# Kernel optimization log

Measured on AMD Instinct MI355X. Metric: run time of the kernel, lower is better.

## Reference

```python
import jax, jax.numpy as jnp
import numpy as np

# pywt db2 decomposition filters
DEC_LO = np.array([-0.12940952255092145, 0.22414386804185735,
                   0.8365163037378079, 0.4829629131445341], dtype=np.float32)
DEC_HI = np.array([-0.4829629131445341, 0.8365163037378079,
                   -0.22414386804185735, -0.12940952255092145], dtype=np.float32)
LEVEL = 3
REC_WEIGHT = 1.0
FILT_LEN = 4
PAD = (2 * FILT_LEN - 3) // 2  # = 2, ptwt reflect padding per side


def _filters(dtype):
    # ptwt uses cross-correlation with flipped pywt filters (== true convolution)
    lo = jnp.asarray(DEC_LO[::-1].copy(), dtype=dtype)
    hi = jnp.asarray(DEC_HI[::-1].copy(), dtype=dtype)
    ll = jnp.outer(lo, lo)  # 'a'
    lh = jnp.outer(hi, lo)  # 'h'
    hl = jnp.outer(lo, hi)  # 'v'
    hh = jnp.outer(hi, hi)  # 'd'
    return jnp.stack([ll, lh, hl, hh])[:, None]  # [4,1,4,4]


def _dwt_step(x, filt):
    # x: [N, nb, H, W] -> [N, 4*nb, H', W'] (each band split into a,h,v,d; grouped)
    n, nb, h, w = x.shape
    padb = PAD + (h % 2)
    padr = PAD + (w % 2)
    xp = jnp.pad(x, ((0, 0), (0, 0), (PAD, padb), (PAD, padr)), mode='reflect')
    k = jnp.tile(filt, (nb, 1, 1, 1))  # [4*nb, 1, 4, 4]
    return jax.lax.conv_general_dilated(
        xp, k, window_strides=(2, 2), padding='VALID',
        feature_group_count=nb,
        dimension_numbers=('NCHW', 'OIHW', 'NCHW'))


def setup_inputs() -> dict:
    key = jax.random.key(0)
    k1, k2 = jax.random.split(key)
    preds = jax.random.normal(k1, (64, 3, 512, 512), dtype=jnp.float32)
    targets = jax.random.normal(k2, (64, 3, 512, 512), dtype=jnp.float32)
    return {"preds": preds, "targets": targets}


def reference(preds, targets):
    n, c, h, w = preds.shape
    p = preds.reshape(n * c, 1, h, w)
    t = targets.reshape(n * c, 1, h, w)
    filt = _filters(preds.dtype)
    for _ in range(LEVEL):
        p = _dwt_step(p, filt)
        t = _dwt_step(t, filt)
    # p, t: [N*C, 4**LEVEL, h', w']; leaf 0 is the all-'a' (pure approx) packet
    per_leaf_mse = jnp.mean((p - t) ** 2, axis=(0, 2, 3))  # [4**LEVEL]
    wvec = jnp.ones(per_leaf_mse.shape[0], dtype=preds.dtype).at[0].set(0.5)
    return REC_WEIGHT * jnp.dot(wvec, per_leaf_mse)
```

## Files before the change

### kernel.cpp

```cpp
#include <hip/hip_runtime.h>

#define F_LO0 0.4829629131445341f
#define F_LO1 0.8365163037378079f
#define F_LO2 0.22414386804185735f
#define F_LO3 (-0.12940952255092145f)
#define F_HI0 (-0.12940952255092145f)
#define F_HI1 (-0.22414386804185735f)
#define F_HI2 0.8365163037378079f
#define F_HI3 (-0.4829629131445341f)

__device__ __forceinline__ int reflect_idx(int r, int n) {
    r = (r < 0) ? -r : r;
    r = (r >= n) ? 2 * n - 2 - r : r;
    return r;
}

__device__ __forceinline__ float4 vfilt(const float4 a, const float4 b,
                                        const float4 c, const float4 d,
                                        float c0, float c1, float c2, float c3) {
    return make_float4(c0 * a.x + c1 * b.x + c2 * c.x + c3 * d.x,
                       c0 * a.y + c1 * b.y + c2 * c.y + c3 * d.y,
                       c0 * a.z + c1 * b.z + c2 * c.z + c3 * d.z,
                       c0 * a.w + c1 * b.w + c2 * c.w + c3 * d.w);
}

__device__ __forceinline__ void hfilt0(const float4 x0, const float4 x1, const float4 x2,
                                       float4& lo, float4& hi) {
    lo.x = F_LO0 * x0.x + F_LO1 * x0.y + F_LO2 * x0.z + F_LO3 * x0.w;
    lo.y = F_LO0 * x0.z + F_LO1 * x0.w + F_LO2 * x1.x + F_LO3 * x1.y;
    lo.z = F_LO0 * x1.x + F_LO1 * x1.y + F_LO2 * x1.z + F_LO3 * x1.w;
    lo.w = F_LO0 * x1.z + F_LO1 * x1.w + F_LO2 * x2.x + F_LO3 * x2.y;
    hi.x = F_HI0 * x0.x + F_HI1 * x0.y + F_HI2 * x0.z + F_HI3 * x0.w;
    hi.y = F_HI0 * x0.z + F_HI1 * x0.w + F_HI2 * x1.x + F_HI3 * x1.y;
    hi.z = F_HI0 * x1.x + F_HI1 * x1.y + F_HI2 * x1.z + F_HI3 * x1.w;
    hi.w = F_HI0 * x1.z + F_HI1 * x1.w + F_HI2 * x2.x + F_HI3 * x2.y;
}

__device__ __forceinline__ void hfilt2(const float4 x0, const float4 x1, const float4 x2,
                                       float4& lo, float4& hi) {
    lo.x = F_LO0 * x0.z + F_LO1 * x0.w + F_LO2 * x1.x + F_LO3 * x1.y;
    lo.y = F_LO0 * x1.x + F_LO1 * x1.y + F_LO2 * x1.z + F_LO3 * x1.w;
    lo.z = F_LO0 * x1.z + F_LO1 * x1.w + F_LO2 * x2.x + F_LO3 * x2.y;
    lo.w = F_LO0 * x2.x + F_LO1 * x2.y + F_LO2 * x2.z + F_LO3 * x2.w;
    hi.x = F_HI0 * x0.z + F_HI1 * x0.w + F_HI2 * x1.x + F_HI3 * x1.y;
    hi.y = F_HI0 * x1.x + F_HI1 * x1.y + F_HI2 * x1.z + F_HI3 * x1.w;
    hi.z = F_HI0 * x1.z + F_HI1 * x1.w + F_HI2 * x2.x + F_HI3 * x2.y;
    hi.w = F_HI0 * x2.x + F_HI1 * x2.y + F_HI2 * x2.z + F_HI3 * x2.w;
}

__global__ void __launch_bounds__(512, 6) k_wpt_fused(
    const float* __restrict__ p, const float* __restrict__ t,
    float* __restrict__ out_sum, float inv_den) {
    constexpr int N0 = 512, N1 = 257, N2 = 130, N3 = 66;

    __shared__ __align__(16) float sA[6240];
    __shared__ __align__(16) float sB[6240];
    __shared__ float wsum[8];

    int bid = blockIdx.x;
    int swz = (bid & 7) * (int)(gridDim.x >> 3) + (bid >> 3);
    int img = swz / 81;
    int tt = swz - img * 81;
    int TA = (tt / 9) * 8;
    int TB = (tt % 9) * 8;

    const int tid = threadIdx.x;
    const size_t ibase = (size_t)img * (N0 * N0);

    const int O0r = 8 * TA - 14, O0c = 8 * TB - 16;
    const int O1r = 4 * TA - 6, O1c = 4 * TB - 6;
    const int O2r = 2 * TA - 2, O2c = 2 * TB - 2;
    const bool edge = (TA == 0) || (TA == 64) || (TB == 0) || (TB == 64);

    if (!edge) {
        const float* __restrict__ pb = p + ibase + (size_t)O0r * N0 + O0c;
        const float* __restrict__ tb = t + ibase + (size_t)O0r * N0 + O0c;
#pragma unroll
        for (int it = 0; it < 4; ++it) {
            int e = it * 512 + tid;
            if (e < 1560) {
                int r = e / 20, q = e - r * 20;
                const float4 pv = *(const float4*)(pb + (size_t)r * N0 + 4 * q);
                const float4 tv = *(const float4*)(tb + (size_t)r * N0 + 4 * q);
                *(float4*)(sA + r * 80 + ((q ^ (r & 1)) << 2)) =
                    make_float4(pv.x - tv.x, pv.y - tv.y, pv.z - tv.z, pv.w - tv.w);
            }
        }
    } else {
#pragma unroll
        for (int it = 0; it < 4; ++it) {
            int e = it * 512 + tid;
            if (e < 1560) {
                int r = e / 20, q = e - r * 20;
                int gr = reflect_idx(O0r + r, N0);
                const float* pr = p + ibase + (size_t)gr * N0;
                const float* tr = t + ibase + (size_t)gr * N0;
                float v[4];
#pragma unroll
                for (int x = 0; x < 4; ++x) {
                    int gc = reflect_idx(O0c + 4 * q + x, N0);
                    v[x] = pr[gc] - tr[gc];
                }
                *(float4*)(sA + r * 80 + ((q ^ (r & 1)) << 2)) =
                    make_float4(v[0], v[1], v[2], v[3]);
            }
        }
    }
    __syncthreads();

#pragma unroll
    for (int it = 0; it < 2; ++it) {
        int e = it * 512 + tid;
        if (e < 780) {
            int r = e / 10, k = e - r * 10;
            int r1 = r & 1;
            const float* row = sA + r * 80;
            int q2 = 2 * k + 2; if (q2 > 19) q2 = 18;
            float4 x0 = *(const float4*)(row + (((2 * k) ^ r1) << 2));
            float4 x1 = *(const float4*)(row + (((2 * k + 1) ^ r1) << 2));
            float4 x2 = *(const float4*)(row + ((q2 ^ r1) << 2));
            float4 lo, hi;
            hfilt2(x0, x1, x2, lo, hi);
            *(float4*)(sB + r * 40 + 4 * k) = lo;
            *(float4*)(sB + 3120 + r * 40 + 4 * k) = hi;
        }
    }
    __syncthreads();

    if (tid < 380) {
        int r1 = tid / 10, k = tid - r1 * 10;
        const float* blo = sB + (2 * r1) * 40 + 4 * k;
        const float* bhi = blo + 3120;
        float4 L0 = *(const float4*)(blo);
        float4 L1v = *(const float4*)(blo + 40);
        float4 L2v = *(const float4*)(blo + 80);
        float4 L3v = *(const float4*)(blo + 120);
        float4 H0 = *(const float4*)(bhi);
        float4 H1 = *(const float4*)(bhi + 40);
        float4 H2 = *(const float4*)(bhi + 80);
        float4 H3 = *(const float4*)(bhi + 120);
        float4 b0 = vfilt(L0, L1v, L2v, L3v, F_LO0, F_LO1, F_LO2, F_LO3);
        float4 b1 = vfilt(L0, L1v, L2v, L3v, F_HI0, F_HI1, F_HI2, F_HI3);
        float4 b2 = vfilt(H0, H1, H2, H3, F_LO0, F_LO1, F_LO2, F_LO3);
        float4 b3 = vfilt(H0, H1, H2, H3, F_HI0, F_HI1, F_HI2, F_HI3);
        int wo = r1 * 40 + ((k ^ (r1 & 1)) << 2);
        *(float4*)(sA + wo) = b0;
        *(float4*)(sA + 1520 + wo) = b1;
        *(float4*)(sA + 3040 + wo) = b2;
        *(float4*)(sA + 4560 + wo) = b3;
    }
    __syncthreads();
    if (edge) {
#pragma unroll
        for (int it = 0; it < 3; ++it) {
            int e = it * 512 + tid;
            if (e < 1444) {
                int lr = e / 38, lc = e - lr * 38;
                int sr = reflect_idx(O1r + lr, N1) - O1r;
                int sc = reflect_idx(O1c + lc, N1) - O1c;
                if ((sr != lr || sc != lc) && (unsigned)sr < 38u && (unsigned)sc < 38u) {
                    int da = lr * 40 + ((((lc >> 2) ^ (lr & 1)) << 2) | (lc & 3));
                    int sa = sr * 40 + ((((sc >> 2) ^ (sr & 1)) << 2) | (sc & 3));
                    sA[da] = sA[sa];
                    sA[1520 + da] = sA[1520 + sa];
                    sA[3040 + da] = sA[3040 + sa];
                    sA[4560 + da] = sA[4560 + sa];
                }
            }
        }
        __syncthreads();
    }

#pragma unroll
    for (int it = 0; it < 2; ++it) {
        int e = it * 512 + tid;
        if (e < 760) {
            int b = e / 190, rem = e - b * 190;
            int r = rem / 5, k = rem - r * 5;
            int r1 = r & 1;
            const float* row = sA + b * 1520 + r * 40;
            int q2 = 2 * k + 2; if (q2 > 9) q2 = 8;
            float4 x0 = *(const float4*)(row + (((2 * k) ^ r1) << 2));
            float4 x1 = *(const float4*)(row + (((2 * k + 1) ^ r1) << 2));
            float4 x2 = *(const float4*)(row + ((q2 ^ r1) << 2));
            float4 lo, hi;
            hfilt0(x0, x1, x2, lo, hi);
            float* dst = sB + b * 1520 + r * 20 + 4 * k;
            *(float4*)dst = lo;
            *(float4*)(dst + 760) = hi;
        }
    }
    __syncthreads();

    if (tid < 360) {
        int b = tid / 90, rem = tid - b * 90;
        int r2 = rem / 5, k = rem - r2 * 5;
        const float* blo = sB + b * 1520 + (2 * r2) * 20 + 4 * k;
        const float* bhi = blo + 760;
        float4 L0 = *(const float4*)(blo);
        float4 L1v = *(const float4*)(blo + 20);
        float4 L2v = *(const float4*)(blo + 40);
        float4 L3v = *(const float4*)(blo + 60);
        float4 H0 = *(const float4*)(bhi);
        float4 H1 = *(const float4*)(bhi + 20);
        float4 H2 = *(const float4*)(bhi + 40);
        float4 H3 = *(const float4*)(bhi + 60);
        float4 b0 = vfilt(L0, L1v, L2v, L3v, F_LO0, F_LO1, F_LO2, F_LO3);
        float4 b1 = vfilt(L0, L1v, L2v, L3v, F_HI0, F_HI1, F_HI2, F_HI3);
        float4 b2 = vfilt(H0, H1, H2, H3, F_LO0, F_LO1, F_LO2, F_LO3);
        float4 b3 = vfilt(H0, H1, H2, H3, F_HI0, F_HI1, F_HI2, F_HI3);
        float* dst = sA + (b * 4) * 360 + r2 * 20 + 4 * k;
        *(float4*)(dst) = b0;
        *(float4*)(dst + 360) = b1;
        *(float4*)(dst + 720) = b2;
        *(float4*)(dst + 1080) = b3;
    }
    __syncthreads();
    if (edge) {
        if (tid < 324) {
            int lr = tid / 18, lc = tid - lr * 18;
            int sr = reflect_idx(O2r + lr, N2) - O2r;
            int sc = reflect_idx(O2c + lc, N2) - O2c;
            if ((sr != lr || sc != lc) && (unsigned)sr < 18u && (unsigned)sc < 18u) {
                int d = lr * 20 + lc;
                int s = sr * 20 + sc;
#pragma unroll
                for (int pp = 0; pp < 16; ++pp) sA[d + 360 * pp] = sA[s + 360 * pp];
            }
        }
        __syncthreads();
    }

#pragma unroll
    for (int it = 0; it < 2; ++it) {
        int e = it * 512 + tid;
        if (e < 576) {
            int pl = e / 36, rem = e - pl * 36;
            int r = rem >> 1, k = rem & 1;
            const float* row = sA + pl * 360 + r * 20 + 8 * k;
            float4 x0 = *(const float4*)(row);
            float4 x1 = *(const float4*)(row + 4);
            float4 x2 = *(const float4*)(row + 8);
            float4 lo, hi;
            hfilt0(x0, x1, x2, lo, hi);
            float* dst = sB + pl * 296 + r * 8 + 4 * k;
            *(float4*)dst = lo;
            *(float4*)(dst + 148) = hi;
        }
    }
    __syncthreads();

    float local = 0.f;
    if (tid < 256) {
        int e = tid;
        int pl = e >> 4;
        int i = (e >> 1) & 7;
        int k = e & 1;
        const float* blo = sB + pl * 296 + (2 * i) * 8 + 4 * k;
        const float* bhi = blo + 148;
        float4 L0 = *(const float4*)(blo);
        float4 L1v = *(const float4*)(blo + 8);
        float4 L2v = *(const float4*)(blo + 16);
        float4 L3v = *(const float4*)(blo + 24);
        float4 H0 = *(const float4*)(bhi);
        float4 H1 = *(const float4*)(bhi + 8);
        float4 H2 = *(const float4*)(bhi + 16);
        float4 H3 = *(const float4*)(bhi + 24);
        float4 o0 = vfilt(L0, L1v, L2v, L3v, F_LO0, F_LO1, F_LO2, F_LO3);
        float4 o1 = vfilt(L0, L1v, L2v, L3v, F_HI0, F_HI1, F_HI2, F_HI3);
        float4 o2 = vfilt(H0, H1, H2, H3, F_LO0, F_LO1, F_LO2, F_LO3);
        float4 o3 = vfilt(H0, H1, H2, H3, F_HI0, F_HI1, F_HI2, F_HI3);
        float w0 = (pl == 0) ? 0.5f : 1.0f;
        int jb = TB + 4 * k;
        if (TA + i < N3) {
            if (jb + 0 < N3) local += w0 * o0.x * o0.x + o1.x * o1.x + o2.x * o2.x + o3.x * o3.x;
            if (jb + 1 < N3) local += w0 * o0.y * o0.y + o1.y * o1.y + o2.y * o2.y + o3.y * o3.y;
            if (jb + 2 < N3) local += w0 * o0.z * o0.z + o1.z * o1.z + o2.z * o2.z + o3.z * o3.z;
            if (jb + 3 < N3) local += w0 * o0.w * o0.w + o1.w * o1.w + o2.w * o2.w + o3.w * o3.w;
        }
    }

#pragma unroll
    for (int off = 32; off > 0; off >>= 1) local += __shfl_down(local, off, 64);
    int wave = tid >> 6;
    if ((tid & 63) == 0) wsum[wave] = local;
    __syncthreads();
    if (tid == 0) {
        float s = 0.f;
#pragma unroll
        for (int w = 0; w < 8; ++w) s += wsum[w];
        atomicAdd(out_sum, s * inv_den);
    }
}

extern "C" void kernel_launch(void* const* d_in, const int* in_sizes, int n_in,
                              void* d_out, int out_size, void* d_ws, size_t ws_size,
                              hipStream_t stream) {
    const float* preds = (const float*)d_in[0];
    const float* targets = (const float*)d_in[1];
    float* out = (float*)d_out;

    hipMemsetAsync(d_out, 0, sizeof(float), stream);

    const float inv_den = 1.0f / (192.0f * 66.0f * 66.0f);
    const int nblk = 192 * 9 * 9;

    k_wpt_fused<<<dim3(nblk), dim3(512), 0, stream>>>(preds, targets, out, inv_den);
}
```

Baseline: 232.2 us.

## Make levels 2-3 wave-private with fused 2D filtering, removing block barriers

The level-2 and level-3 transforms are restructured so each wavefront owns one level-1 band and half its rows. It computes the full 2D separable filter, horizontal then vertical, in registers and writes to a per-wave scratch region. Edge reflection and the final level run inside the wave, which removes several block-wide __syncthreads and the intermediate horizontal-pass buffers. The cost is redundant horizontal filtering for overlapping rows and a larger shared buffer. The XOR swizzle on the level-1 layout is dropped, which may add LDS bank conflicts.

```diff
diff --git a/kernel.cpp b/kernel.cpp
--- a/kernel.cpp
+++ b/kernel.cpp
@@ -22,18 +22,6 @@
                        c0 * a.y + c1 * b.y + c2 * c.y + c3 * d.y,
                        c0 * a.z + c1 * b.z + c2 * c.z + c3 * d.z,
                        c0 * a.w + c1 * b.w + c2 * c.w + c3 * d.w);
-}
-
-__device__ __forceinline__ void hfilt0(const float4 x0, const float4 x1, const float4 x2,
-                                       float4& lo, float4& hi) {
-    lo.x = F_LO0 * x0.x + F_LO1 * x0.y + F_LO2 * x0.z + F_LO3 * x0.w;
-    lo.y = F_LO0 * x0.z + F_LO1 * x0.w + F_LO2 * x1.x + F_LO3 * x1.y;
-    lo.z = F_LO0 * x1.x + F_LO1 * x1.y + F_LO2 * x1.z + F_LO3 * x1.w;
-    lo.w = F_LO0 * x1.z + F_LO1 * x1.w + F_LO2 * x2.x + F_LO3 * x2.y;
-    hi.x = F_HI0 * x0.x + F_HI1 * x0.y + F_HI2 * x0.z + F_HI3 * x0.w;
-    hi.y = F_HI0 * x0.z + F_HI1 * x0.w + F_HI2 * x1.x + F_HI3 * x1.y;
-    hi.z = F_HI0 * x1.x + F_HI1 * x1.y + F_HI2 * x1.z + F_HI3 * x1.w;
-    hi.w = F_HI0 * x1.z + F_HI1 * x1.w + F_HI2 * x2.x + F_HI3 * x2.y;
 }
 
 __device__ __forceinline__ void hfilt2(const float4 x0, const float4 x1, const float4 x2,
@@ -54,7 +42,7 @@
     constexpr int N0 = 512, N1 = 257, N2 = 130, N3 = 66;
 
     __shared__ __align__(16) float sA[6240];
-    __shared__ __align__(16) float sB[6240];
+    __shared__ __align__(16) float sB[6912];
     __shared__ float wsum[8];
 
     int bid = blockIdx.x;
@@ -143,7 +131,7 @@
         float4 b1 = vfilt(L0, L1v, L2v, L3v, F_HI0, F_HI1, F_HI2, F_HI3);
         float4 b2 = vfilt(H0, H1, H2, H3, F_LO0, F_LO1, F_LO2, F_LO3);
         float4 b3 = vfilt(H0, H1, H2, H3, F_HI0, F_HI1, F_HI2, F_HI3);
-        int wo = r1 * 40 + ((k ^ (r1 & 1)) << 2);
+        int wo = r1 * 40 + 4 * k;
         *(float4*)(sA + wo) = b0;
         *(float4*)(sA + 1520 + wo) = b1;
         *(float4*)(sA + 3040 + wo) = b2;
@@ -159,8 +147,8 @@
                 int sr = reflect_idx(O1r + lr, N1) - O1r;
                 int sc = reflect_idx(O1c + lc, N1) - O1c;
                 if ((sr != lr || sc != lc) && (unsigned)sr < 38u && (unsigned)sc < 38u) {
-                    int da = lr * 40 + ((((lc >> 2) ^ (lr & 1)) << 2) | (lc & 3));
-                    int sa = sr * 40 + ((((sc >> 2) ^ (sr & 1)) << 2) | (sc & 3));
+                    int da = lr * 40 + lc;
+                    int sa = sr * 40 + sc;
                     sA[da] = sA[sa];
                     sA[1520 + da] = sA[1520 + sa];
                     sA[3040 + da] = sA[3040 + sa];
@@ -171,125 +159,93 @@
         __syncthreads();
     }
 
-#pragma unroll
-    for (int it = 0; it < 2; ++it) {
-        int e = it * 512 + tid;
-        if (e < 760) {
-            int b = e / 190, rem = e - b * 190;
-            int r = rem / 5, k = rem - r * 5;
-            int r1 = r & 1;
-            const float* row = sA + b * 1520 + r * 40;
-            int q2 = 2 * k + 2; if (q2 > 9) q2 = 8;
-            float4 x0 = *(const float4*)(row + (((2 * k) ^ r1) << 2));
-            float4 x1 = *(const float4*)(row + (((2 * k + 1) ^ r1) << 2));
-            float4 x2 = *(const float4*)(row + ((q2 ^ r1) << 2));
-            float4 lo, hi;
-            hfilt0(x0, x1, x2, lo, hi);
-            float* dst = sB + b * 1520 + r * 20 + 4 * k;
-            *(float4*)dst = lo;
-            *(float4*)(dst + 760) = hi;
-        }
-    }
-    __syncthreads();
-
-    if (tid < 360) {
-        int b = tid / 90, rem = tid - b * 90;
-        int r2 = rem / 5, k = rem - r2 * 5;
-        const float* blo = sB + b * 1520 + (2 * r2) * 20 + 4 * k;
-        const float* bhi = blo + 760;
-        float4 L0 = *(const float4*)(blo);
-        float4 L1v = *(const float4*)(blo + 20);
-        float4 L2v = *(const float4*)(blo + 40);
-        float4 L3v = *(const float4*)(blo + 60);
-        float4 H0 = *(const float4*)(bhi);
-        float4 H1 = *(const float4*)(bhi + 20);
-        float4 H2 = *(const float4*)(bhi + 40);
-        float4 H3 = *(const float4*)(bhi + 60);
-        float4 b0 = vfilt(L0, L1v, L2v, L3v, F_LO0, F_LO1, F_LO2, F_LO3);
-        float4 b1 = vfilt(L0, L1v, L2v, L3v, F_HI0, F_HI1, F_HI2, F_HI3);
-        float4 b2 = vfilt(H0, H1, H2, H3, F_LO0, F_LO1, F_LO2, F_LO3);
-        float4 b3 = vfilt(H0, H1, H2, H3, F_HI0, F_HI1, F_HI2, F_HI3);
-        float* dst = sA + (b * 4) * 360 + r2 * 20 + 4 * k;
-        *(float4*)(dst) = b0;
-        *(float4*)(dst + 360) = b1;
-        *(float4*)(dst + 720) = b2;
-        *(float4*)(dst + 1080) = b3;
-    }
-    __syncthreads();
+    const int w = tid >> 6;
+    const int ln = tid & 63;
+    const int bnd = w >> 1;
+    const int hf = w & 1;
+    const int off = hf * 6;
+    float* scr = sB + w * 864;
+    const float* L1b = sA + bnd * 1520;
+
+    if (ln < 54) {
+        const int c = ln % 18, s = ln / 18;
+#pragma unroll
+        for (int tq = 0; tq < 4; ++tq) {
+            const int r2l = 3 * tq + s;
+            const float* base = L1b + (2 * (off + r2l)) * 40 + 2 * c;
+            float lo[4], hi[4];
+#pragma unroll
+            for (int u = 0; u < 4; ++u) {
+                float2 a = *(const float2*)(base + u * 40);
+                float2 d = *(const float2*)(base + u * 40 + 2);
+                lo[u] = F_LO0 * a.x + F_LO1 * a.y + F_LO2 * d.x + F_LO3 * d.y;
+                hi[u] = F_HI0 * a.x + F_HI1 * a.y + F_HI2 * d.x + F_HI3 * d.y;
+            }
+            int sl = r2l * 18 + c;
+            scr[sl]       = F_LO0 * lo[0] + F_LO1 * lo[1] + F_LO2 * lo[2] + F_LO3 * lo[3];
+            scr[sl + 216] = F_HI0 * lo[0] + F_HI1 * lo[1] + F_HI2 * lo[2] + F_HI3 * lo[3];
+            scr[sl + 432] = F_LO0 * hi[0] + F_LO1 * hi[1] + F_LO2 * hi[2] + F_LO3 * hi[3];
+            scr[sl + 648] = F_HI0 * hi[0] + F_HI1 * hi[1] + F_HI2 * hi[2] + F_HI3 * hi[3];
+        }
+    }
+
     if (edge) {
-        if (tid < 324) {
-            int lr = tid / 18, lc = tid - lr * 18;
-            int sr = reflect_idx(O2r + lr, N2) - O2r;
-            int sc = reflect_idx(O2c + lc, N2) - O2c;
-            if ((sr != lr || sc != lc) && (unsigned)sr < 18u && (unsigned)sc < 18u) {
-                int d = lr * 20 + lc;
-                int s = sr * 20 + sc;
-#pragma unroll
-                for (int pp = 0; pp < 16; ++pp) sA[d + 360 * pp] = sA[s + 360 * pp];
-            }
-        }
-        __syncthreads();
-    }
-
-#pragma unroll
-    for (int it = 0; it < 2; ++it) {
-        int e = it * 512 + tid;
-        if (e < 576) {
-            int pl = e / 36, rem = e - pl * 36;
-            int r = rem >> 1, k = rem & 1;
-            const float* row = sA + pl * 360 + r * 20 + 8 * k;
-            float4 x0 = *(const float4*)(row);
-            float4 x1 = *(const float4*)(row + 4);
-            float4 x2 = *(const float4*)(row + 8);
-            float4 lo, hi;
-            hfilt0(x0, x1, x2, lo, hi);
-            float* dst = sB + pl * 296 + r * 8 + 4 * k;
-            *(float4*)dst = lo;
-            *(float4*)(dst + 148) = hi;
-        }
-    }
-    __syncthreads();
+#pragma unroll
+        for (int q = 0; q < 4; ++q) {
+            int e = q * 54 + ln;
+            if (ln < 54 && e < 216) {
+                int lr = e / 18, lc = e - lr * 18;
+                int srt = reflect_idx(O2r + off + lr, N2) - O2r - off;
+                int sct = reflect_idx(O2c + lc, N2) - O2c;
+                if ((srt != lr || sct != lc) &&
+                    (unsigned)srt < 12u && (unsigned)sct < 18u) {
+                    int d = lr * 18 + lc, sidx = srt * 18 + sct;
+#pragma unroll
+                    for (int pl = 0; pl < 4; ++pl)
+                        scr[d + 216 * pl] = scr[sidx + 216 * pl];
+                }
+            }
+        }
+    }
 
     float local = 0.f;
-    if (tid < 256) {
-        int e = tid;
-        int pl = e >> 4;
-        int i = (e >> 1) & 7;
-        int k = e & 1;
-        const float* blo = sB + pl * 296 + (2 * i) * 8 + 4 * k;
-        const float* bhi = blo + 148;
-        float4 L0 = *(const float4*)(blo);
-        float4 L1v = *(const float4*)(blo + 8);
-        float4 L2v = *(const float4*)(blo + 16);
-        float4 L3v = *(const float4*)(blo + 24);
-        float4 H0 = *(const float4*)(bhi);
-        float4 H1 = *(const float4*)(bhi + 8);
-        float4 H2 = *(const float4*)(bhi + 16);
-        float4 H3 = *(const float4*)(bhi + 24);
-        float4 o0 = vfilt(L0, L1v, L2v, L3v, F_LO0, F_LO1, F_LO2, F_LO3);
-        float4 o1 = vfilt(L0, L1v, L2v, L3v, F_HI0, F_HI1, F_HI2, F_HI3);
-        float4 o2 = vfilt(H0, H1, H2, H3, F_LO0, F_LO1, F_LO2, F_LO3);
-        float4 o3 = vfilt(H0, H1, H2, H3, F_HI0, F_HI1, F_HI2, F_HI3);
-        float w0 = (pl == 0) ? 0.5f : 1.0f;
-        int jb = TB + 4 * k;
-        if (TA + i < N3) {
-            if (jb + 0 < N3) local += w0 * o0.x * o0.x + o1.x * o1.x + o2.x * o2.x + o3.x * o3.x;
-            if (jb + 1 < N3) local += w0 * o0.y * o0.y + o1.y * o1.y + o2.y * o2.y + o3.y * o3.y;
-            if (jb + 2 < N3) local += w0 * o0.z * o0.z + o1.z * o1.z + o2.z * o2.z + o3.z * o3.z;
-            if (jb + 3 < N3) local += w0 * o0.w * o0.w + o1.w * o1.w + o2.w * o2.w + o3.w * o3.w;
-        }
-    }
-
-#pragma unroll
-    for (int off = 32; off > 0; off >>= 1) local += __shfl_down(local, off, 64);
-    int wave = tid >> 6;
-    if ((tid & 63) == 0) wsum[wave] = local;
+    {
+        const int pp = ln >> 5, rem = ln & 31, r3 = rem >> 3, j = rem & 7;
+        const int i = hf * 4 + r3;
+        const int sr0 = 2 * r3 + hf * 2;
+        const bool valid = (TA + i < N3) && (TB + j < N3);
+#pragma unroll
+        for (int pi = 0; pi < 2; ++pi) {
+            const int pl = 2 * pp + pi;
+            const float* pb = scr + pl * 216 + sr0 * 18 + 2 * j;
+            float lo[4], hi[4];
+#pragma unroll
+            for (int u = 0; u < 4; ++u) {
+                float2 a = *(const float2*)(pb + u * 18);
+                float2 d = *(const float2*)(pb + u * 18 + 2);
+                lo[u] = F_LO0 * a.x + F_LO1 * a.y + F_LO2 * d.x + F_LO3 * d.y;
+                hi[u] = F_HI0 * a.x + F_HI1 * a.y + F_HI2 * d.x + F_HI3 * d.y;
+            }
+            float o0 = F_LO0 * lo[0] + F_LO1 * lo[1] + F_LO2 * lo[2] + F_LO3 * lo[3];
+            float o1 = F_HI0 * lo[0] + F_HI1 * lo[1] + F_HI2 * lo[2] + F_HI3 * lo[3];
+            float o2 = F_LO0 * hi[0] + F_LO1 * hi[1] + F_LO2 * hi[2] + F_LO3 * hi[3];
+            float o3 = F_HI0 * hi[0] + F_HI1 * hi[1] + F_HI2 * hi[2] + F_HI3 * hi[3];
+            if (valid) {
+                float w00 = (bnd == 0 && pl == 0) ? 0.5f : 1.0f;
+                local += w00 * o0 * o0 + o1 * o1 + o2 * o2 + o3 * o3;
+            }
+        }
+    }
+
+#pragma unroll
+    for (int o = 32; o > 0; o >>= 1) local += __shfl_down(local, o, 64);
+    if (ln == 0) wsum[w] = local;
     __syncthreads();
     if (tid == 0) {
-        float s = 0.f;
-#pragma unroll
-        for (int w = 0; w < 8; ++w) s += wsum[w];
-        atomicAdd(out_sum, s * inv_den);
+        float ssum = 0.f;
+#pragma unroll
+        for (int x = 0; x < 8; ++x) ssum += wsum[x];
+        atomicAdd(out_sum, ssum * inv_den);
     }
 }
 
```

New measurement: 232.6 us. No clear change (+0.2%).
